# Kernel tuning notes

Hardware: AMD Instinct MI355X
Metric: run time of the kernel (lower is better)

The kernel has to match this reference:

```python
import jax, jax.numpy as jnp
import numpy as np

D_MODEL = 2048
D_FF = 8192
N_HEADS = 16
N_KV_HEADS = 8
HEAD_DIM = D_MODEL // N_HEADS  # 128
R_Q = 64
R_KV = 64
KERNEL_DIM = 64
LN_EPS = 1e-5


def setup_inputs() -> dict:
    key = jax.random.key(0)
    ks = jax.random.split(key, 16)
    s = 0.02
    inp = {
        "x": jax.random.normal(ks[0], (4, 4096, D_MODEL), dtype=jnp.float32),
        # multi-latent low-rank projections (stored as (in, out))
        "W_dq": jax.random.normal(ks[1], (D_MODEL, R_Q), dtype=jnp.float32) * s,
        "W_uq": jax.random.normal(ks[2], (R_Q, N_HEADS * HEAD_DIM), dtype=jnp.float32) * s,
        "W_dkv": jax.random.normal(ks[3], (D_MODEL, R_KV), dtype=jnp.float32) * s,
        "W_uk": jax.random.normal(ks[4], (R_KV, N_KV_HEADS * HEAD_DIM), dtype=jnp.float32) * s,
        "W_uv": jax.random.normal(ks[5], (R_KV, N_KV_HEADS * HEAD_DIM), dtype=jnp.float32) * s,
        # laplacian kernel random features: omega ~ Cauchy (random Fourier features of Laplacian kernel)
        "omega": jax.random.cauchy(ks[6], (HEAD_DIM, KERNEL_DIM), dtype=jnp.float32) * 0.1,
        "W_o": jax.random.normal(ks[7], (N_HEADS * HEAD_DIM, D_MODEL), dtype=jnp.float32) * s,
        "ln1_g": jnp.ones((D_MODEL,), jnp.float32),
        "ln1_b": jnp.zeros((D_MODEL,), jnp.float32),
        "gate_W": jax.random.normal(ks[8], (D_MODEL, D_FF), dtype=jnp.float32) * s,
        "up_W": jax.random.normal(ks[9], (D_MODEL, D_FF), dtype=jnp.float32) * s,
        "down_W": jax.random.normal(ks[10], (D_FF, D_MODEL), dtype=jnp.float32) * s,
        "ln2_g": jnp.ones((D_MODEL,), jnp.float32),
        "ln2_b": jnp.zeros((D_MODEL,), jnp.float32),
    }
    return inp


def _layernorm(x, g, b):
    mu = jnp.mean(x, axis=-1, keepdims=True)
    var = jnp.var(x, axis=-1, keepdims=True)
    return (x - mu) * jax.lax.rsqrt(var + LN_EPS) * g + b


def _phi(x, omega):
    # laplacian-kernel random Fourier feature map: [B,H,S,Dh] -> [B,H,S,2*KERNEL_DIM]
    proj = jnp.einsum("bhsd,dk->bhsk", x, omega)
    scale = 1.0 / jnp.sqrt(jnp.float32(KERNEL_DIM))
    return jnp.concatenate([jnp.cos(proj), jnp.sin(proj)], axis=-1) * scale


def _mlgka_forward(x, W_dq, W_uq, W_dkv, W_uk, W_uv, omega, W_o,
                   ln1_g, ln1_b, gate_W, up_W, down_W, ln2_g, ln2_b):
    B, S, _ = x.shape
    # --- multi-latent (low-rank) Q/KV projections ---
    c_q = jnp.einsum("bsd,dr->bsr", x, W_dq)            # [B,S,r_q]
    q = jnp.einsum("bsr,re->bse", c_q, W_uq)            # [B,S,H*Dh]
    c_kv = jnp.einsum("bsd,dr->bsr", x, W_dkv)          # [B,S,r_kv]
    k = jnp.einsum("bsr,re->bse", c_kv, W_uk)           # [B,S,Hkv*Dh]
    v = jnp.einsum("bsr,re->bse", c_kv, W_uv)           # [B,S,Hkv*Dh]

    q = q.reshape(B, S, N_HEADS, HEAD_DIM).transpose(0, 2, 1, 3)        # [B,H,S,Dh]
    k = k.reshape(B, S, N_KV_HEADS, HEAD_DIM).transpose(0, 2, 1, 3)     # [B,Hkv,S,Dh]
    v = v.reshape(B, S, N_KV_HEADS, HEAD_DIM).transpose(0, 2, 1, 3)

    # GQA: repeat kv heads to match query heads
    rep = N_HEADS // N_KV_HEADS
    k = jnp.repeat(k, rep, axis=1)                                      # [B,H,S,Dh]
    v = jnp.repeat(v, rep, axis=1)

    # --- kernelized (linear) bidirectional attention ---
    phi_q = _phi(q, omega)                                              # [B,H,S,F]
    phi_k = _phi(k, omega)                                              # [B,H,S,F]
    kv = jnp.einsum("bhsf,bhsd->bhfd", phi_k, v)                        # [B,H,F,Dh]
    z = jnp.sum(phi_k, axis=2)                                          # [B,H,F]
    num = jnp.einsum("bhsf,bhfd->bhsd", phi_q, kv)                      # [B,H,S,Dh]
    den = jnp.einsum("bhsf,bhf->bhs", phi_q, z)[..., None]              # [B,H,S,1]
    attn = num / (den + 1e-6)

    attn = attn.transpose(0, 2, 1, 3).reshape(B, S, N_HEADS * HEAD_DIM)
    attn_out = jnp.einsum("bse,ed->bsd", attn, W_o)

    # --- residual + LN, SwiGLU FFN, residual + LN ---
    h = _layernorm(x + attn_out, ln1_g, ln1_b)
    gate = jnp.einsum("bsd,df->bsf", h, gate_W)
    up = jnp.einsum("bsd,df->bsf", h, up_W)
    ffn = jnp.einsum("bsf,fd->bsd", gate * jax.nn.silu(up), down_W)
    return _layernorm(h + ffn, ln2_g, ln2_b)


def reference(x, W_dq, W_uq, W_dkv, W_uk, W_uv, omega, W_o,
              ln1_g, ln1_b, gate_W, up_W, down_W, ln2_g, ln2_b):
    return _mlgka_forward(x, W_dq, W_uq, W_dkv, W_uk, W_uv, omega, W_o,
                          ln1_g, ln1_b, gate_W, up_W, down_W, ln2_g, ln2_b)
```

## Files before the change

kernel.cpp:

```cpp
#include <hip/hip_runtime.h>
#include <stdint.h>
#include <math.h>


typedef __bf16 bf16x8 __attribute__((ext_vector_type(8)));
typedef float f32x4 __attribute__((ext_vector_type(4)));
typedef float f32x2 __attribute__((ext_vector_type(2)));
typedef unsigned short u16x8 __attribute__((ext_vector_type(8)));
typedef unsigned short u16x4 __attribute__((ext_vector_type(4)));

#define DEV __device__ __forceinline__

DEV unsigned short f2b(float f) {
  union { float f; unsigned int u; } v;
  v.f = f;
  unsigned int u = v.u;
  return (unsigned short)((u + 0x7FFFu + ((u >> 16) & 1u)) >> 16);
}
DEV float b2f(unsigned short h) {
  union { unsigned int u; float f; } v;
  v.u = ((unsigned int)h) << 16;
  return v.f;
}

DEV void async16(const void* g, void* l) {
  typedef __attribute__((address_space(1))) unsigned int* gp_t;
  typedef __attribute__((address_space(3))) unsigned int* lp_t;
  __builtin_amdgcn_global_load_lds((gp_t)(g), (lp_t)(l), 16, 0, 0);
}

#define SCHED0() __builtin_amdgcn_sched_barrier(0)
#define BARRIER() do { SCHED0(); __builtin_amdgcn_s_barrier(); SCHED0(); } while (0)
#define LGKM0() do { asm volatile("s_waitcnt lgkmcnt(0)" ::: "memory"); SCHED0(); } while (0)

template <int BN, typename Epi>
DEV void gemm8p(const unsigned short* __restrict__ A,
                const unsigned short* __restrict__ Bt,
                int K, int lda, int ldb, Epi epi) {
  constexpr int CW = BN / 4;
  constexpr int JT = CW / 32;
  constexpr int QBS = CW / 2;
  constexpr int SZB = BN * 64;
  constexpr int BUFB = 2 * 16384 + 2 * SZB;
  constexpr int LB = BN / 128;
  constexpr int VMC = 4 + LB;
  __shared__ alignas(16) char lds[2 * BUFB];

  const int tid = threadIdx.x;
  const int lane = tid & 63;
  const int wave = tid >> 6;
  const int wm = wave >> 2, wn = wave & 3;
  const int ln = lane & 15;
  const int kq2 = ((lane >> 4) & 3) << 4;

  int srA[2], kbA[2], srB[2], kbB[2];
#pragma unroll
  for (int p = 0; p < 2; ++p) {
    int o = (p * 512 + tid) * 16;
    int x = o ^ (((o >> 9) & 1) << 5);
    srA[p] = x >> 7; kbA[p] = (x & 127) >> 1;
  }
#pragma unroll
  for (int p = 0; p < LB; ++p) {
    int o = (p * 512 + tid) * 16;
    int x = o ^ (((o >> 9) & 1) << 5);
    srB[p] = x >> 7; kbB[p] = (x & 127) >> 1;
  }

  const int NT = K >> 6;

  auto stageA = [&](int T, int qa) {
    char* dst = lds + (T & 1) * BUFB + qa * 16384;
    const unsigned short* src = A + T * 64;
#pragma unroll
    for (int p = 0; p < 2; ++p) {
      int r = ((srA[p] >> 6) << 7) | (qa << 6) | (srA[p] & 63);
      async16(src + (size_t)r * lda + kbA[p], dst + (p * 512 + tid) * 16);
    }
  };
  auto stageB = [&](int T, int qb) {
    char* dst = lds + (T & 1) * BUFB + 32768 + qb * SZB;
    const unsigned short* src = Bt + T * 64;
#pragma unroll
    for (int p = 0; p < LB; ++p) {
      int n = (srB[p] / QBS) * CW + qb * QBS + (srB[p] % QBS);
      async16(src + (size_t)n * ldb + kbB[p], dst + (p * 512 + tid) * 16);
    }
  };

  bf16x8 av[4][2], bv[JT][2];
  auto readA = [&](int b, int qa) {
#pragma unroll
    for (int i = 0; i < 4; ++i) {
      int sr = wm * 64 + i * 16 + ln;
      const char* rp = lds + b * BUFB + qa * 16384 + sr * 128;
      int sw = (sr & 4) << 3;
      av[i][0] = *(const bf16x8*)(rp + (kq2 ^ sw));
      av[i][1] = *(const bf16x8*)(rp + ((64 + kq2) ^ sw));
    }
  };
  auto readB = [&](int b, int qb) {
#pragma unroll
    for (int j = 0; j < JT; ++j) {
      int sr = wn * QBS + j * 16 + ln;
      const char* rp = lds + b * BUFB + 32768 + qb * SZB + sr * 128;
      int sw = (sr & 4) << 3;
      bv[j][0] = *(const bf16x8*)(rp + (kq2 ^ sw));
      bv[j][1] = *(const bf16x8*)(rp + ((64 + kq2) ^ sw));
    }
  };

  f32x4 acc[8][2 * JT];
  const f32x4 fz = {0.f, 0.f, 0.f, 0.f};
#pragma unroll
  for (int i = 0; i < 8; ++i)
#pragma unroll
    for (int j = 0; j < 2 * JT; ++j) acc[i][j] = fz;

  auto mf = [&](int qa, int qb) {
#pragma unroll
    for (int tt = 0; tt < 2; ++tt)
#pragma unroll
      for (int i = 0; i < 4; ++i)
#pragma unroll
        for (int j = 0; j < JT; ++j)
          acc[qa * 4 + i][qb * JT + j] = __builtin_amdgcn_mfma_f32_16x16x32_bf16(
              av[i][tt], bv[j][tt], acc[qa * 4 + i][qb * JT + j], 0, 0, 0);
  };

  auto vwait_steady = [&]() {
    if constexpr (VMC == 6) asm volatile("s_waitcnt vmcnt(6)" ::: "memory");
    else                    asm volatile("s_waitcnt vmcnt(5)" ::: "memory");
  };

  stageA(0, 0); stageB(0, 0); stageB(0, 1); stageA(0, 1);
  if (NT > 1) {
    stageA(1, 0); stageB(1, 1); stageA(1, 1);
    vwait_steady();
  } else {
    asm volatile("s_waitcnt vmcnt(0)" ::: "memory");
  }
  BARRIER();

  for (int t = 0; t < NT; ++t) {
    const int b = t & 1;
    readA(b, 0); readB(b, 0);
    if (t + 1 < NT) stageB(t + 1, 0);
    BARRIER(); LGKM0();
    __builtin_amdgcn_s_setprio(1); mf(0, 0); __builtin_amdgcn_s_setprio(0);
    BARRIER();
    readB(b, 1);
    if (t + 2 < NT) stageA(t + 2, 0);
    BARRIER(); LGKM0();
    __builtin_amdgcn_s_setprio(1); mf(0, 1); __builtin_amdgcn_s_setprio(0);
    BARRIER();
    readA(b, 1);
    if (t + 2 < NT) stageB(t + 2, 1);
    BARRIER(); LGKM0();
    __builtin_amdgcn_s_setprio(1); mf(1, 1); __builtin_amdgcn_s_setprio(0);
    BARRIER();
    readB(b, 0);
    if (t + 2 < NT) stageA(t + 2, 1);
    BARRIER(); LGKM0();
    __builtin_amdgcn_s_setprio(1); mf(1, 0); __builtin_amdgcn_s_setprio(0);
    if (t + 2 < NT) vwait_steady();
    else            asm volatile("s_waitcnt vmcnt(0)" ::: "memory");
    BARRIER();
  }

  const int rb = ((lane >> 4) & 3) * 4;
#pragma unroll
  for (int qa = 0; qa < 2; ++qa)
#pragma unroll
    for (int i = 0; i < 4; ++i)
#pragma unroll
      for (int qb = 0; qb < 2; ++qb)
#pragma unroll
        for (int j = 0; j < JT; ++j)
#pragma unroll
          for (int r = 0; r < 4; ++r)
            epi(wm * 128 + qa * 64 + i * 16 + rb + r,
                wn * CW + qb * QBS + j * 16 + ln,
                acc[qa * 4 + i][qb * JT + j][r]);
}

__global__ __launch_bounds__(512) void k_gemm_wo(const unsigned short* __restrict__ A,
                                                 const unsigned short* __restrict__ Bt,
                                                 const float* __restrict__ x,
                                                 unsigned short* __restrict__ y) {
  const int bid = blockIdx.x;
  const int swz = (bid & 7) * 64 + (bid >> 3);
  const int m0 = (swz >> 3) * 256, n0 = (swz & 7) * 256;
  gemm8p<256>(A + (size_t)m0 * 2048, Bt + (size_t)n0 * 2048, 2048, 2048, 2048,
              [=](int r, int cc, float v) {
                size_t idx = (size_t)(m0 + r) * 2048 + n0 + cc;
                y[idx] = f2b(v + x[idx]);
              });
}

__global__ __launch_bounds__(512) void k_gemm_up2(const unsigned short* __restrict__ A,
                                                  const unsigned short* __restrict__ Bt,
                                                  unsigned short* __restrict__ act) {
  const int bid = blockIdx.x;
  const int swz = (bid & 7) * 64 + (bid >> 3);
  const int m0 = (swz >> 5) * 256, n0 = (swz & 31) * 256;
  gemm8p<256>(A + (size_t)m0 * 2048, Bt + (size_t)n0 * 2048, 2048, 2048, 2048,
              [=](int r, int cc, float v) {
                float s = v / (1.f + __expf(-v));
                act[(size_t)(m0 + r) * 8192 + n0 + cc] = f2b(s);
              });
}

__global__ __launch_bounds__(512) void k_gemm_gatem(const unsigned short* __restrict__ A,
                                                    const unsigned short* __restrict__ Bt,
                                                    unsigned short* act) {
  const int bid = blockIdx.x;
  const int swz = (bid & 7) * 64 + (bid >> 3);
  const int m0 = (swz >> 5) * 256, n0 = (swz & 31) * 256;
  gemm8p<256>(A + (size_t)m0 * 2048, Bt + (size_t)n0 * 2048, 2048, 2048, 2048,
              [=](int r, int cc, float v) {
                size_t idx = (size_t)(m0 + r) * 8192 + n0 + cc;
                act[idx] = f2b(v * b2f(act[idx]));
              });
}

__global__ __launch_bounds__(512) void k_gemm_down2(const unsigned short* __restrict__ A,
                                                    const unsigned short* __restrict__ Bt,
                                                    const unsigned short* __restrict__ hbuf,
                                                    float* __restrict__ outc) {
  const int bid = blockIdx.x;
  const int swz = (bid & 7) * 32 + (bid >> 3);
  const int m0 = (swz >> 4) * 256, n0 = (swz & 15) * 128;
  gemm8p<128>(A + (size_t)m0 * 8192, Bt + (size_t)n0 * 8192, 8192, 8192, 8192,
              [=](int r, int cc, float v) {
                size_t idx = (size_t)(m0 + r) * 2048 + n0 + cc;
                outc[idx] = v + b2f(hbuf[idx]);
              });
}

__global__ __launch_bounds__(256) void k_tc(const float* __restrict__ in,
                                            unsigned short* __restrict__ out, int R, int C) {
  __shared__ float tile[64][65];
  const int c0 = blockIdx.x * 64, r0 = blockIdx.y * 64;
  const int tid = threadIdx.x;
#pragma unroll
  for (int p = 0; p < 16; ++p) {
    int l = p * 256 + tid;
    int ir = l >> 6, ic = l & 63;
    tile[ic][ir] = in[(size_t)(r0 + ir) * C + c0 + ic];
  }
  __syncthreads();
#pragma unroll
  for (int p = 0; p < 16; ++p) {
    int l = p * 256 + tid;
    int oc = l >> 6, orr = l & 63;
    out[(size_t)(c0 + oc) * R + r0 + orr] = f2b(tile[oc][orr]);
  }
}

__global__ __launch_bounds__(256) void k_zero(float* __restrict__ p, int n) {
  int i = blockIdx.x * 256 + threadIdx.x;
  if (i < n) p[i] = 0.f;
}

__global__ __launch_bounds__(256) void k_wproj(const float* __restrict__ W_uq,
                                               const float* __restrict__ W_uk,
                                               const float* __restrict__ omega,
                                               float* __restrict__ wqp, float* __restrict__ wkp) {
  const int bi = blockIdx.x;
  const float* W;
  float* outp;
  int ldw, col0;
  if (bi < 16) { W = W_uq; outp = wqp + bi * 4096; ldw = 2048; col0 = bi * 128; }
  else         { W = W_uk; outp = wkp + (bi - 16) * 4096; ldw = 1024; col0 = (bi - 16) * 128; }
  __shared__ float om[128][64];
  const int tid = threadIdx.x;
#pragma unroll
  for (int p = 0; p < 32; ++p) {
    int l = p * 256 + tid;
    om[l >> 6][l & 63] = omega[l];
  }
  __syncthreads();
  const int r = tid >> 2, f0 = (tid & 3) * 16;
  float acc[16];
#pragma unroll
  for (int f = 0; f < 16; ++f) acc[f] = 0.f;
  const float* wrow = W + (size_t)r * ldw + col0;
  for (int d = 0; d < 128; ++d) {
    float w = wrow[d];
#pragma unroll
    for (int f = 0; f < 16; ++f) acc[f] += w * om[d][f0 + f];
  }
#pragma unroll
  for (int f = 0; f < 16; ++f) outp[r * 64 + f0 + f] = acc[f];
}

__global__ __launch_bounds__(256) void k_cgemm(const float* __restrict__ x,
                                               const float* __restrict__ W_dq,
                                               const float* __restrict__ W_dkv,
                                               float* __restrict__ cbuf) {
  __shared__ float xs[64][65];
  __shared__ float wsh[64][128];
  const int tok0 = blockIdx.x * 64;
  const int tid = threadIdx.x;
  const int ty = tid >> 3, tx = tid & 7;
  const int t0 = ty * 2, c0 = tx * 16;
  float acc[2][16];
#pragma unroll
  for (int i = 0; i < 2; ++i)
#pragma unroll
    for (int e = 0; e < 16; ++e) acc[i][e] = 0.f;
  for (int kb = 0; kb < 2048; kb += 64) {
#pragma unroll
    for (int p = 0; p < 16; ++p) {
      int l = p * 256 + tid;
      int tr = l >> 6, kd = l & 63;
      xs[tr][kd] = x[(size_t)(tok0 + tr) * 2048 + kb + kd];
    }
#pragma unroll
    for (int p = 0; p < 32; ++p) {
      int l = p * 256 + tid;
      int kd = l >> 7, c = l & 127;
      wsh[kd][c] = (c < 64) ? W_dq[(size_t)(kb + kd) * 64 + c]
                            : W_dkv[(size_t)(kb + kd) * 64 + (c - 64)];
    }
    __syncthreads();
    for (int kd = 0; kd < 64; ++kd) {
      float a0 = xs[t0][kd], a1 = xs[t0 + 1][kd];
#pragma unroll
      for (int e = 0; e < 16; ++e) {
        float w = wsh[kd][c0 + e];
        acc[0][e] += a0 * w;
        acc[1][e] += a1 * w;
      }
    }
    __syncthreads();
  }
#pragma unroll
  for (int i = 0; i < 2; ++i)
#pragma unroll
    for (int e = 0; e < 16; ++e)
      cbuf[(size_t)(tok0 + t0 + i) * 128 + c0 + e] = acc[i][e];
}

__global__ __launch_bounds__(256) void k_phikz(const float* __restrict__ c,
                                               const float* __restrict__ wkp,
                                               float* __restrict__ phikT,
                                               float* __restrict__ z) {
  const int s0 = blockIdx.x * 64;
  const int bh = blockIdx.y;
  const int b = bh >> 3, hkv = bh & 7;
  __shared__ float ck[64][65];
  __shared__ float wp[64][68];
  const int tid = threadIdx.x;
#pragma unroll
  for (int p = 0; p < 16; ++p) {
    int l = p * 256 + tid;
    int sr = l >> 6, d = l & 63;
    ck[sr][d] = c[(size_t)(b * 4096 + s0 + sr) * 128 + 64 + d];
    wp[sr][d] = wkp[hkv * 4096 + l];
  }
  __syncthreads();
  const int ty = tid & 31, fx = tid >> 5;
  const int f0 = fx * 8, r0 = ty * 2;
  float pr[2][8];
#pragma unroll
  for (int rr = 0; rr < 2; ++rr)
#pragma unroll
    for (int ff = 0; ff < 8; ++ff) pr[rr][ff] = 0.f;
  for (int d = 0; d < 64; ++d) {
    f32x4 w0 = *(const f32x4*)&wp[d][f0];
    f32x4 w1 = *(const f32x4*)&wp[d][f0 + 4];
    float c0v = ck[r0][d], c1v = ck[r0 + 1][d];
#pragma unroll
    for (int e = 0; e < 4; ++e) {
      pr[0][e] += c0v * w0[e]; pr[0][4 + e] += c0v * w1[e];
      pr[1][e] += c1v * w0[e]; pr[1][4 + e] += c1v * w1[e];
    }
  }
  float* obase = phikT + (size_t)bh * 524288 + s0 + r0;
  float zc[8], zs2[8];
#pragma unroll
  for (int ff = 0; ff < 8; ++ff) {
    float sv0, cv0, sv1, cv1;
    __sincosf(pr[0][ff], &sv0, &cv0);
    __sincosf(pr[1][ff], &sv1, &cv1);
    float c0 = cv0 * 0.125f, c1 = cv1 * 0.125f;
    float s0v = sv0 * 0.125f, s1v = sv1 * 0.125f;
    f32x2 co; co[0] = c0; co[1] = c1;
    f32x2 si; si[0] = s0v; si[1] = s1v;
    *(f32x2*)(obase + (size_t)(f0 + ff) * 4096) = co;
    *(f32x2*)(obase + (size_t)(64 + f0 + ff) * 4096) = si;
    zc[ff] = c0 + c1;
    zs2[ff] = s0v + s1v;
  }
#pragma unroll
  for (int off = 16; off; off >>= 1) {
#pragma unroll
    for (int ff = 0; ff < 8; ++ff) {
      zc[ff] += __shfl_down(zc[ff], off);
      zs2[ff] += __shfl_down(zs2[ff], off);
    }
  }
  if (ty == 0) {
#pragma unroll
    for (int ff = 0; ff < 8; ++ff) {
      atomicAdd(&z[bh * 128 + f0 + ff], zc[ff]);
      atomicAdd(&z[bh * 128 + 64 + f0 + ff], zs2[ff]);
    }
  }
}

__global__ __launch_bounds__(256) void k_vf(const float* __restrict__ c,
                                            const float* __restrict__ W_uv,
                                            float* __restrict__ vT) {
  const int s0 = blockIdx.x * 64;
  const int bh = blockIdx.y;
  const int b = bh >> 3, hkv = bh & 7;
  __shared__ float ck[64][65];
  __shared__ float wv[64][132];
  const int tid = threadIdx.x;
#pragma unroll
  for (int p = 0; p < 16; ++p) {
    int l = p * 256 + tid;
    int sr = l >> 6, d = l & 63;
    ck[sr][d] = c[(size_t)(b * 4096 + s0 + sr) * 128 + 64 + d];
  }
#pragma unroll
  for (int p = 0; p < 32; ++p) {
    int l = p * 256 + tid;
    int rr = l >> 7, d = l & 127;
    wv[rr][d] = W_uv[(size_t)rr * 1024 + hkv * 128 + d];
  }
  __syncthreads();
  const int ty = tid & 15, tx = tid >> 4;
  const int r0 = ty * 4, d0 = tx * 8;
  float acc[4][8];
#pragma unroll
  for (int rr = 0; rr < 4; ++rr)
#pragma unroll
    for (int dd = 0; dd < 8; ++dd) acc[rr][dd] = 0.f;
  for (int kk = 0; kk < 64; ++kk) {
    f32x4 w0 = *(const f32x4*)&wv[kk][d0];
    f32x4 w1 = *(const f32x4*)&wv[kk][d0 + 4];
    float cv[4];
#pragma unroll
    for (int rr = 0; rr < 4; ++rr) cv[rr] = ck[r0 + rr][kk];
#pragma unroll
    for (int rr = 0; rr < 4; ++rr)
#pragma unroll
      for (int e = 0; e < 4; ++e) {
        acc[rr][e] += cv[rr] * w0[e];
        acc[rr][4 + e] += cv[rr] * w1[e];
      }
  }
  float* obase = vT + (size_t)bh * 524288 + s0 + r0;
#pragma unroll
  for (int dd = 0; dd < 8; ++dd) {
    f32x4 pv;
    pv[0] = acc[0][dd]; pv[1] = acc[1][dd]; pv[2] = acc[2][dd]; pv[3] = acc[3][dd];
    *(f32x4*)(obase + (size_t)(d0 + dd) * 4096) = pv;
  }
}

__global__ __launch_bounds__(256) void k_kvf2(const float* __restrict__ phikT,
                                              const float* __restrict__ vT,
                                              float* __restrict__ kvf) {
  const int fq = blockIdx.x >> 2, dq = blockIdx.x & 3, bh = blockIdx.y;
  const float* pT = phikT + (size_t)bh * 524288 + (size_t)fq * 32 * 4096;
  const float* vB = vT + (size_t)bh * 524288 + (size_t)dq * 32 * 4096;
  __shared__ float ps[64][33];
  __shared__ float vs[64][33];
  const int tid = threadIdx.x;
  const int fi = tid >> 3, d0 = (tid & 7) * 4;
  f32x4 acc = {0.f, 0.f, 0.f, 0.f};
  for (int ss = 0; ss < 4096; ss += 64) {
#pragma unroll
    for (int p = 0; p < 8; ++p) {
      int l = p * 256 + tid;
      int rr = l >> 6, si = l & 63;
      ps[si][rr] = pT[(size_t)rr * 4096 + ss + si];
      vs[si][rr] = vB[(size_t)rr * 4096 + ss + si];
    }
    __syncthreads();
    for (int si = 0; si < 64; ++si) {
      float pv = ps[si][fi];
#pragma unroll
      for (int j = 0; j < 4; ++j) acc[j] += pv * vs[si][d0 + j];
    }
    __syncthreads();
  }
  float* o = kvf + ((size_t)bh * 128 + fq * 32 + fi) * 128 + dq * 32 + d0;
  *(f32x4*)o = acc;
}

__global__ __launch_bounds__(256) void k_attn2(const float* __restrict__ c,
                                               const float* __restrict__ wqp,
                                               const float* __restrict__ zb,
                                               const float* __restrict__ kvf,
                                               unsigned short* __restrict__ attn) {
  const int s0 = blockIdx.x * 64;
  const int bh = blockIdx.y;
  const int b = bh >> 4, hh = bh & 15;
  const int bhk = (b << 3) + (hh >> 1);
  __shared__ float wq[4096];
  __shared__ float cqt[64][33];
  __shared__ float phl[32][130];
  __shared__ float kvl[128][32];
  __shared__ float zl[128];
  __shared__ float denl[32];
  const int tid = threadIdx.x;
  if (tid < 128) zl[tid] = zb[bhk * 128 + tid];
#pragma unroll
  for (int p = 0; p < 16; ++p) wq[p * 256 + tid] = wqp[hh * 4096 + p * 256 + tid];
  const int fx = tid & 7, ty = tid >> 3;
  const int f0 = fx * 8;
  for (int hf = 0; hf < 2; ++hf) {
    __syncthreads();
#pragma unroll
    for (int p = 0; p < 8; ++p) {
      int l = p * 256 + tid;
      int sr = l >> 6, dd = l & 63;
      cqt[dd][sr] = c[(size_t)(b * 4096 + s0 + hf * 32 + sr) * 128 + dd];
    }
    __syncthreads();
    float pr[8];
#pragma unroll
    for (int ff = 0; ff < 8; ++ff) pr[ff] = 0.f;
    for (int dd = 0; dd < 64; ++dd) {
      f32x4 w0 = *(const f32x4*)(wq + dd * 64 + f0);
      f32x4 w1 = *(const f32x4*)(wq + dd * 64 + f0 + 4);
      float cv = cqt[dd][ty];
#pragma unroll
      for (int e = 0; e < 4; ++e) { pr[e] += cv * w0[e]; pr[4 + e] += cv * w1[e]; }
    }
    float dpart = 0.f;
#pragma unroll
    for (int ff = 0; ff < 8; ++ff) {
      float sv, cv;
      __sincosf(pr[ff], &sv, &cv);
      cv *= 0.125f; sv *= 0.125f;
      phl[ty][f0 + ff] = cv;
      phl[ty][64 + f0 + ff] = sv;
      dpart += cv * zl[f0 + ff] + sv * zl[64 + f0 + ff];
    }
    dpart += __shfl_down(dpart, 4);
    dpart += __shfl_down(dpart, 2);
    dpart += __shfl_down(dpart, 1);
    if (fx == 0) denl[ty] = dpart + 1e-6f;
    __syncthreads();
    for (int dq = 0; dq < 4; ++dq) {
#pragma unroll
      for (int p = 0; p < 16; ++p) {
        int l = p * 256 + tid;
        int f = l >> 5, j = l & 31;
        kvl[f][j] = kvf[(size_t)bhk * 16384 + (size_t)f * 128 + dq * 32 + j];
      }
      __syncthreads();
      const int row = tid >> 3, d0 = (tid & 7) * 4;
      f32x4 acc = {0.f, 0.f, 0.f, 0.f};
      for (int f = 0; f < 128; f += 2) {
        f32x2 pa = *(const f32x2*)&phl[row][f];
        f32x4 k0 = *(const f32x4*)&kvl[f][d0];
        f32x4 k1 = *(const f32x4*)&kvl[f + 1][d0];
#pragma unroll
        for (int j = 0; j < 4; ++j) acc[j] += pa[0] * k0[j] + pa[1] * k1[j];
      }
      const float dn = denl[row];
      u16x4 o4;
#pragma unroll
      for (int j = 0; j < 4; ++j) o4[j] = f2b(acc[j] / dn);
      *(u16x4*)(attn + (size_t)(b * 4096 + s0 + hf * 32 + row) * 2048 + hh * 128 + dq * 32 + d0) = o4;
      __syncthreads();
    }
  }
}

__global__ __launch_bounds__(256) void k_ln_b2b(const unsigned short* __restrict__ in,
                                                const float* __restrict__ g,
                                                const float* __restrict__ bb,
                                                unsigned short* __restrict__ ob) {
  const int row = blockIdx.x;
  const unsigned short* xr = in + (size_t)row * 2048;
  float vals[8], s = 0.f, ss = 0.f;
#pragma unroll
  for (int i = 0; i < 8; ++i) {
    float v = b2f(xr[i * 256 + threadIdx.x]);
    vals[i] = v; s += v; ss += v * v;
  }
#pragma unroll
  for (int off = 32; off; off >>= 1) { s += __shfl_down(s, off); ss += __shfl_down(ss, off); }
  __shared__ float red[8];
  const int wave = threadIdx.x >> 6;
  if ((threadIdx.x & 63) == 0) { red[wave * 2] = s; red[wave * 2 + 1] = ss; }
  __syncthreads();
  float S = red[0] + red[2] + red[4] + red[6];
  float SS = red[1] + red[3] + red[5] + red[7];
  float mu = S * (1.f / 2048.f);
  float var = SS * (1.f / 2048.f) - mu * mu;
  float inv = rsqrtf(var + 1e-5f);
#pragma unroll
  for (int i = 0; i < 8; ++i) {
    int col = i * 256 + threadIdx.x;
    ob[(size_t)row * 2048 + col] = f2b((vals[i] - mu) * inv * g[col] + bb[col]);
  }
}

__global__ __launch_bounds__(256) void k_ln_ip(float* __restrict__ io,
                                               const float* __restrict__ g,
                                               const float* __restrict__ bb) {
  const int row = blockIdx.x;
  float* xr = io + (size_t)row * 2048;
  float vals[8], s = 0.f, ss = 0.f;
#pragma unroll
  for (int i = 0; i < 8; ++i) {
    float v = xr[i * 256 + threadIdx.x];
    vals[i] = v; s += v; ss += v * v;
  }
#pragma unroll
  for (int off = 32; off; off >>= 1) { s += __shfl_down(s, off); ss += __shfl_down(ss, off); }
  __shared__ float red[8];
  const int wave = threadIdx.x >> 6;
  if ((threadIdx.x & 63) == 0) { red[wave * 2] = s; red[wave * 2 + 1] = ss; }
  __syncthreads();
  float S = red[0] + red[2] + red[4] + red[6];
  float SS = red[1] + red[3] + red[5] + red[7];
  float mu = S * (1.f / 2048.f);
  float var = SS * (1.f / 2048.f) - mu * mu;
  float inv = rsqrtf(var + 1e-5f);
#pragma unroll
  for (int i = 0; i < 8; ++i) {
    int col = i * 256 + threadIdx.x;
    xr[col] = (vals[i] - mu) * inv * g[col] + bb[col];
  }
}

extern "C" void kernel_launch(void* const* d_in, const int* in_sizes, int n_in,
                              void* d_out, int out_size, void* d_ws, size_t ws_size,
                              hipStream_t stream) {
  (void)in_sizes; (void)n_in; (void)out_size; (void)ws_size;
  const float* x     = (const float*)d_in[0];
  const float* W_dq  = (const float*)d_in[1];
  const float* W_uq  = (const float*)d_in[2];
  const float* W_dkv = (const float*)d_in[3];
  const float* W_uk  = (const float*)d_in[4];
  const float* W_uv  = (const float*)d_in[5];
  const float* omega = (const float*)d_in[6];
  const float* W_o   = (const float*)d_in[7];
  const float* ln1g  = (const float*)d_in[8];
  const float* ln1b  = (const float*)d_in[9];
  const float* gateW = (const float*)d_in[10];
  const float* upW   = (const float*)d_in[11];
  const float* downW = (const float*)d_in[12];
  const float* ln2g  = (const float*)d_in[13];
  const float* ln2b  = (const float*)d_in[14];
  float* out = (float*)d_out;

  char* w = (char*)d_ws;
  float*          phikTf = (float*)(w);
  float*          vTf    = (float*)(w + 67108864);
  unsigned short* attn   = (unsigned short*)(w + 67108864);
  unsigned short* hb     = (unsigned short*)(w + 67108864);
  unsigned short* gatet  = (unsigned short*)(w);
  unsigned short* upt    = (unsigned short*)(w + 33554432);
  char* C = w + 134217728;
  float*          cbuf = (float*)(C);
  float*          wqp  = (float*)(C + 8388608);
  float*          wkp  = (float*)(C + 8650752);
  float*          zb   = (float*)(C + 8781824);
  float*          kvf  = (float*)(C + 8798208);
  unsigned short* y    = (unsigned short*)(C);
  unsigned short* act  = (unsigned short*)(C);
  unsigned short* wot   = (unsigned short*)(w + 201326592);
  unsigned short* downt = (unsigned short*)(w + 209715200);

  k_zero<<<16, 256, 0, stream>>>(zb, 4096);
  k_wproj<<<24, 256, 0, stream>>>(W_uq, W_uk, omega, wqp, wkp);
  k_tc<<<dim3(32, 32), 256, 0, stream>>>(W_o, wot, 2048, 2048);

  k_cgemm<<<256, 256, 0, stream>>>(x, W_dq, W_dkv, cbuf);

  k_phikz<<<dim3(64, 32), 256, 0, stream>>>(cbuf, wkp, phikTf, zb);
  k_vf<<<dim3(64, 32), 256, 0, stream>>>(cbuf, W_uv, vTf);

  k_kvf2<<<dim3(16, 32), 256, 0, stream>>>(phikTf, vTf, kvf);
  k_attn2<<<dim3(64, 64), 256, 0, stream>>>(cbuf, wqp, zb, kvf, attn);

  k_gemm_wo<<<dim3(512), 512, 0, stream>>>(attn, wot, x, y);
  k_ln_b2b<<<16384, 256, 0, stream>>>(y, ln1g, ln1b, hb);

  k_tc<<<dim3(128, 32), 256, 0, stream>>>(gateW, gatet, 2048, 8192);
  k_tc<<<dim3(128, 32), 256, 0, stream>>>(upW, upt, 2048, 8192);
  k_tc<<<dim3(32, 128), 256, 0, stream>>>(downW, downt, 8192, 2048);

  for (int cix = 0; cix < 4; ++cix) {
    const unsigned short* hbc = hb + (size_t)cix * 4096 * 2048;
    float* outc = out + (size_t)cix * 4096 * 2048;
    k_gemm_up2<<<dim3(512), 512, 0, stream>>>(hbc, upt, act);
    k_gemm_gatem<<<dim3(512), 512, 0, stream>>>(hbc, gatet, act);
    k_gemm_down2<<<dim3(256), 512, 0, stream>>>(act, downt, hbc, outc);
    k_ln_ip<<<4096, 256, 0, stream>>>(outc, ln2g, ln2b);
  }
}
```

Baseline: 3.160 ms.

## Move linear-attention KV and numerator products onto bf16 MFMA GEMMs

Stores phi_k and v as bf16 instead of fp32 and replaces the scalar fp32 kv reduction with a split-K bf16 MFMA GEMM, followed by a reduce-and-transpose kernel. The attention kernel is split in two: one computes phi_q in bf16 plus reciprocal denominators, the other runs the phi_q·kv numerator as an MFMA GEMM with scaling in the epilogue. The aim is to take the attention stage off slow scalar FMA loops and halve intermediate traffic. The cost is extra launches, partial-sum buffers, and bf16 rounding of phi and kv.

```diff
diff --git a/kernel.cpp b/kernel.cpp
--- a/kernel.cpp
+++ b/kernel.cpp
@@ -8,6 +8,7 @@
 typedef float f32x2 __attribute__((ext_vector_type(2)));
 typedef unsigned short u16x8 __attribute__((ext_vector_type(8)));
 typedef unsigned short u16x4 __attribute__((ext_vector_type(4)));
+typedef unsigned short u16x2 __attribute__((ext_vector_type(2)));
 
 #define DEV __device__ __forceinline__
 
@@ -32,6 +33,64 @@
 #define SCHED0() __builtin_amdgcn_sched_barrier(0)
 #define BARRIER() do { SCHED0(); __builtin_amdgcn_s_barrier(); SCHED0(); } while (0)
 #define LGKM0() do { asm volatile("s_waitcnt lgkmcnt(0)" ::: "memory"); SCHED0(); } while (0)
+
+template <typename Epi>
+DEV void gemm_core(const unsigned short* __restrict__ A,
+                   const unsigned short* __restrict__ Bt,
+                   int K, int lda, int ldb, Epi epi) {
+  __shared__ alignas(16) unsigned short As[128 * 64];
+  __shared__ alignas(16) unsigned short Bs[128 * 64];
+  const int tid = threadIdx.x;
+  const int lane = tid & 63;
+  const int wr = ((tid >> 6) >> 1) * 64;
+  const int wc = ((tid >> 6) & 1) * 64;
+  const int ln = lane & 15;
+  const int kq = (lane >> 4) * 8;
+
+  const f32x4 fz = {0.f, 0.f, 0.f, 0.f};
+  f32x4 acc[4][4];
+#pragma unroll
+  for (int i = 0; i < 4; ++i)
+#pragma unroll
+    for (int j = 0; j < 4; ++j) acc[i][j] = fz;
+
+  for (int kb = 0; kb < K; kb += 64) {
+#pragma unroll
+    for (int c = 0; c < 4; ++c) {
+      int o = (c * 256 + tid) * 16;
+      int row = o >> 7;
+      int ke = (o & 127) >> 1;
+      async16(A + (size_t)row * lda + kb + ke, (void*)(As + (o >> 1)));
+      async16(Bt + (size_t)row * ldb + kb + ke, (void*)(Bs + (o >> 1)));
+    }
+    __syncthreads();
+#pragma unroll
+    for (int t = 0; t < 2; ++t) {
+      const int kk = t * 32 + kq;
+      bf16x8 av[4], bv[4];
+#pragma unroll
+      for (int i = 0; i < 4; ++i)
+        av[i] = *(const bf16x8*)(As + (wr + i * 16 + ln) * 64 + kk);
+#pragma unroll
+      for (int j = 0; j < 4; ++j)
+        bv[j] = *(const bf16x8*)(Bs + (wc + j * 16 + ln) * 64 + kk);
+#pragma unroll
+      for (int i = 0; i < 4; ++i)
+#pragma unroll
+        for (int j = 0; j < 4; ++j)
+          acc[i][j] = __builtin_amdgcn_mfma_f32_16x16x32_bf16(av[i], bv[j], acc[i][j], 0, 0, 0);
+    }
+    __syncthreads();
+  }
+  const int rb = (lane >> 4) * 4;
+#pragma unroll
+  for (int i = 0; i < 4; ++i)
+#pragma unroll
+    for (int j = 0; j < 4; ++j)
+#pragma unroll
+      for (int r = 0; r < 4; ++r)
+        epi(wr + i * 16 + rb + r, wc + j * 16 + ln, acc[i][j][r]);
+}
 
 template <int BN, typename Epi>
 DEV void gemm8p(const unsigned short* __restrict__ A,
@@ -345,7 +404,7 @@
 
 __global__ __launch_bounds__(256) void k_phikz(const float* __restrict__ c,
                                                const float* __restrict__ wkp,
-                                               float* __restrict__ phikT,
+                                               unsigned short* __restrict__ phikT,
                                                float* __restrict__ z) {
   const int s0 = blockIdx.x * 64;
   const int bh = blockIdx.y;
@@ -378,7 +437,7 @@
       pr[1][e] += c1v * w0[e]; pr[1][4 + e] += c1v * w1[e];
     }
   }
-  float* obase = phikT + (size_t)bh * 524288 + s0 + r0;
+  unsigned short* obase = phikT + (size_t)bh * 524288 + s0 + r0;
   float zc[8], zs2[8];
 #pragma unroll
   for (int ff = 0; ff < 8; ++ff) {
@@ -387,10 +446,10 @@
     __sincosf(pr[1][ff], &sv1, &cv1);
     float c0 = cv0 * 0.125f, c1 = cv1 * 0.125f;
     float s0v = sv0 * 0.125f, s1v = sv1 * 0.125f;
-    f32x2 co; co[0] = c0; co[1] = c1;
-    f32x2 si; si[0] = s0v; si[1] = s1v;
-    *(f32x2*)(obase + (size_t)(f0 + ff) * 4096) = co;
-    *(f32x2*)(obase + (size_t)(64 + f0 + ff) * 4096) = si;
+    u16x2 co; co[0] = f2b(c0); co[1] = f2b(c1);
+    u16x2 si; si[0] = f2b(s0v); si[1] = f2b(s1v);
+    *(u16x2*)(obase + (size_t)(f0 + ff) * 4096) = co;
+    *(u16x2*)(obase + (size_t)(64 + f0 + ff) * 4096) = si;
     zc[ff] = c0 + c1;
     zs2[ff] = s0v + s1v;
   }
@@ -413,7 +472,7 @@
 
 __global__ __launch_bounds__(256) void k_vf(const float* __restrict__ c,
                                             const float* __restrict__ W_uv,
-                                            float* __restrict__ vT) {
+                                            unsigned short* __restrict__ vT) {
   const int s0 = blockIdx.x * 64;
   const int bh = blockIdx.y;
   const int b = bh >> 3, hkv = bh & 7;
@@ -454,61 +513,63 @@
         acc[rr][4 + e] += cv[rr] * w1[e];
       }
   }
-  float* obase = vT + (size_t)bh * 524288 + s0 + r0;
+  unsigned short* obase = vT + (size_t)bh * 524288 + s0 + r0;
 #pragma unroll
   for (int dd = 0; dd < 8; ++dd) {
-    f32x4 pv;
-    pv[0] = acc[0][dd]; pv[1] = acc[1][dd]; pv[2] = acc[2][dd]; pv[3] = acc[3][dd];
-    *(f32x4*)(obase + (size_t)(d0 + dd) * 4096) = pv;
-  }
-}
-
-__global__ __launch_bounds__(256) void k_kvf2(const float* __restrict__ phikT,
-                                              const float* __restrict__ vT,
-                                              float* __restrict__ kvf) {
-  const int fq = blockIdx.x >> 2, dq = blockIdx.x & 3, bh = blockIdx.y;
-  const float* pT = phikT + (size_t)bh * 524288 + (size_t)fq * 32 * 4096;
-  const float* vB = vT + (size_t)bh * 524288 + (size_t)dq * 32 * 4096;
-  __shared__ float ps[64][33];
-  __shared__ float vs[64][33];
-  const int tid = threadIdx.x;
-  const int fi = tid >> 3, d0 = (tid & 7) * 4;
-  f32x4 acc = {0.f, 0.f, 0.f, 0.f};
-  for (int ss = 0; ss < 4096; ss += 64) {
-#pragma unroll
-    for (int p = 0; p < 8; ++p) {
-      int l = p * 256 + tid;
-      int rr = l >> 6, si = l & 63;
-      ps[si][rr] = pT[(size_t)rr * 4096 + ss + si];
-      vs[si][rr] = vB[(size_t)rr * 4096 + ss + si];
-    }
-    __syncthreads();
-    for (int si = 0; si < 64; ++si) {
-      float pv = ps[si][fi];
-#pragma unroll
-      for (int j = 0; j < 4; ++j) acc[j] += pv * vs[si][d0 + j];
-    }
-    __syncthreads();
-  }
-  float* o = kvf + ((size_t)bh * 128 + fq * 32 + fi) * 128 + dq * 32 + d0;
-  *(f32x4*)o = acc;
-}
-
-__global__ __launch_bounds__(256) void k_attn2(const float* __restrict__ c,
-                                               const float* __restrict__ wqp,
-                                               const float* __restrict__ zb,
-                                               const float* __restrict__ kvf,
-                                               unsigned short* __restrict__ attn) {
+    u16x4 pv;
+    pv[0] = f2b(acc[0][dd]); pv[1] = f2b(acc[1][dd]);
+    pv[2] = f2b(acc[2][dd]); pv[3] = f2b(acc[3][dd]);
+    *(u16x4*)(obase + (size_t)(d0 + dd) * 4096) = pv;
+  }
+}
+
+__global__ __launch_bounds__(256) void k_kvg(const unsigned short* __restrict__ phikT,
+                                             const unsigned short* __restrict__ vT,
+                                             float* __restrict__ kvp) {
+  const int kc = blockIdx.x, bh = blockIdx.y;
+  gemm_core(phikT + (size_t)bh * 524288 + kc * 512,
+            vT + (size_t)bh * 524288 + kc * 512, 512, 4096, 4096,
+            [=](int r, int cc, float v) {
+              kvp[((size_t)(kc * 32 + bh) * 128 + r) * 128 + cc] = v;
+            });
+}
+
+__global__ __launch_bounds__(256) void k_kvredt(const float* __restrict__ kvp,
+                                                unsigned short* __restrict__ kvbT) {
+  const int fx0 = blockIdx.x * 64, dx0 = blockIdx.y * 64, bhk = blockIdx.z;
+  __shared__ float tile[64][65];
+  const int tid = threadIdx.x;
+#pragma unroll
+  for (int p = 0; p < 16; ++p) {
+    int l = p * 256 + tid;
+    int fr = l >> 6, dc = l & 63;
+    float s = 0.f;
+#pragma unroll
+    for (int kc = 0; kc < 8; ++kc)
+      s += kvp[(size_t)kc * 524288 + ((size_t)bhk * 128 + fx0 + fr) * 128 + dx0 + dc];
+    tile[dc][fr] = s;
+  }
+  __syncthreads();
+#pragma unroll
+  for (int p = 0; p < 16; ++p) {
+    int l = p * 256 + tid;
+    int dr = l >> 6, fc = l & 63;
+    kvbT[((size_t)bhk * 128 + dx0 + dr) * 128 + fx0 + fc] = f2b(tile[dr][fc]);
+  }
+}
+
+__global__ __launch_bounds__(256) void k_phiq(const float* __restrict__ c,
+                                              const float* __restrict__ wqp,
+                                              const float* __restrict__ zb,
+                                              unsigned short* __restrict__ phiq,
+                                              float* __restrict__ rden) {
   const int s0 = blockIdx.x * 64;
   const int bh = blockIdx.y;
   const int b = bh >> 4, hh = bh & 15;
   const int bhk = (b << 3) + (hh >> 1);
   __shared__ float wq[4096];
   __shared__ float cqt[64][33];
-  __shared__ float phl[32][130];
-  __shared__ float kvl[128][32];
   __shared__ float zl[128];
-  __shared__ float denl[32];
   const int tid = threadIdx.x;
   if (tid < 128) zl[tid] = zb[bhk * 128 + tid];
 #pragma unroll
@@ -535,45 +596,39 @@
       for (int e = 0; e < 4; ++e) { pr[e] += cv * w0[e]; pr[4 + e] += cv * w1[e]; }
     }
     float dpart = 0.f;
+    u16x8 pc, ps;
 #pragma unroll
     for (int ff = 0; ff < 8; ++ff) {
       float sv, cv;
       __sincosf(pr[ff], &sv, &cv);
       cv *= 0.125f; sv *= 0.125f;
-      phl[ty][f0 + ff] = cv;
-      phl[ty][64 + f0 + ff] = sv;
+      pc[ff] = f2b(cv); ps[ff] = f2b(sv);
       dpart += cv * zl[f0 + ff] + sv * zl[64 + f0 + ff];
     }
+    unsigned short* ob = phiq + ((size_t)bh * 4096 + s0 + hf * 32 + ty) * 128;
+    *(u16x8*)(ob + f0) = pc;
+    *(u16x8*)(ob + 64 + f0) = ps;
     dpart += __shfl_down(dpart, 4);
     dpart += __shfl_down(dpart, 2);
     dpart += __shfl_down(dpart, 1);
-    if (fx == 0) denl[ty] = dpart + 1e-6f;
-    __syncthreads();
-    for (int dq = 0; dq < 4; ++dq) {
-#pragma unroll
-      for (int p = 0; p < 16; ++p) {
-        int l = p * 256 + tid;
-        int f = l >> 5, j = l & 31;
-        kvl[f][j] = kvf[(size_t)bhk * 16384 + (size_t)f * 128 + dq * 32 + j];
-      }
-      __syncthreads();
-      const int row = tid >> 3, d0 = (tid & 7) * 4;
-      f32x4 acc = {0.f, 0.f, 0.f, 0.f};
-      for (int f = 0; f < 128; f += 2) {
-        f32x2 pa = *(const f32x2*)&phl[row][f];
-        f32x4 k0 = *(const f32x4*)&kvl[f][d0];
-        f32x4 k1 = *(const f32x4*)&kvl[f + 1][d0];
-#pragma unroll
-        for (int j = 0; j < 4; ++j) acc[j] += pa[0] * k0[j] + pa[1] * k1[j];
-      }
-      const float dn = denl[row];
-      u16x4 o4;
-#pragma unroll
-      for (int j = 0; j < 4; ++j) o4[j] = f2b(acc[j] / dn);
-      *(u16x4*)(attn + (size_t)(b * 4096 + s0 + hf * 32 + row) * 2048 + hh * 128 + dq * 32 + d0) = o4;
-      __syncthreads();
-    }
-  }
+    if (fx == 0) rden[(size_t)bh * 4096 + s0 + hf * 32 + ty] = 1.f / (dpart + 1e-6f);
+  }
+}
+
+__global__ __launch_bounds__(256) void k_num(const unsigned short* __restrict__ phiq,
+                                             const unsigned short* __restrict__ kvbT,
+                                             const float* __restrict__ rden,
+                                             unsigned short* __restrict__ attn) {
+  const int m0 = blockIdx.x * 128;
+  const int bh = blockIdx.y;
+  const int b = bh >> 4, hh = bh & 15;
+  const int bhk = (b << 3) + (hh >> 1);
+  const float* rd = rden + (size_t)bh * 4096 + m0;
+  gemm_core(phiq + ((size_t)bh * 4096 + m0) * 128, kvbT + (size_t)bhk * 16384,
+            128, 128, 128,
+            [=](int r, int cc, float v) {
+              attn[(size_t)(b * 4096 + m0 + r) * 2048 + hh * 128 + cc] = f2b(v * rd[r]);
+            });
 }
 
 __global__ __launch_bounds__(256) void k_ln_b2b(const unsigned short* __restrict__ in,
@@ -657,18 +712,21 @@
   float* out = (float*)d_out;
 
   char* w = (char*)d_ws;
-  float*          phikTf = (float*)(w);
-  float*          vTf    = (float*)(w + 67108864);
-  unsigned short* attn   = (unsigned short*)(w + 67108864);
-  unsigned short* hb     = (unsigned short*)(w + 67108864);
-  unsigned short* gatet  = (unsigned short*)(w);
-  unsigned short* upt    = (unsigned short*)(w + 33554432);
+  unsigned short* phikT = (unsigned short*)(w);
+  unsigned short* phiqb = (unsigned short*)(w);
+  unsigned short* vT    = (unsigned short*)(w + 67108864);
+  unsigned short* attn  = (unsigned short*)(w + 67108864);
+  unsigned short* hb    = (unsigned short*)(w + 67108864);
+  unsigned short* gatet = (unsigned short*)(w);
+  unsigned short* upt   = (unsigned short*)(w + 33554432);
   char* C = w + 134217728;
   float*          cbuf = (float*)(C);
   float*          wqp  = (float*)(C + 8388608);
   float*          wkp  = (float*)(C + 8650752);
   float*          zb   = (float*)(C + 8781824);
-  float*          kvf  = (float*)(C + 8798208);
+  float*          rden = (float*)(C + 8798208);
+  unsigned short* kvbT = (unsigned short*)(C + 9846784);
+  float*          kvp  = (float*)(C + 10895360);
   unsigned short* y    = (unsigned short*)(C);
   unsigned short* act  = (unsigned short*)(C);
   unsigned short* wot   = (unsigned short*)(w + 201326592);
@@ -680,11 +738,13 @@
 
   k_cgemm<<<256, 256, 0, stream>>>(x, W_dq, W_dkv, cbuf);
 
-  k_phikz<<<dim3(64, 32), 256, 0, stream>>>(cbuf, wkp, phikTf, zb);
-  k_vf<<<dim3(64, 32), 256, 0, stream>>>(cbuf, W_uv, vTf);
-
-  k_kvf2<<<dim3(16, 32), 256, 0, stream>>>(phikTf, vTf, kvf);
-  k_attn2<<<dim3(64, 64), 256, 0, stream>>>(cbuf, wqp, zb, kvf, attn);
+  k_phikz<<<dim3(64, 32), 256, 0, stream>>>(cbuf, wkp, phikT, zb);
+  k_vf<<<dim3(64, 32), 256, 0, stream>>>(cbuf, W_uv, vT);
+
+  k_kvg<<<dim3(8, 32), 256, 0, stream>>>(phikT, vT, kvp);
+  k_kvredt<<<dim3(2, 2, 32), 256, 0, stream>>>(kvp, kvbT);
+  k_phiq<<<dim3(64, 64), 256, 0, stream>>>(cbuf, wqp, zb, phiqb, rden);
+  k_num<<<dim3(32, 64), 256, 0, stream>>>(phiqb, kvbT, rden, attn);
 
   k_gemm_wo<<<dim3(512), 512, 0, stream>>>(attn, wot, x, y);
   k_ln_b2b<<<16384, 256, 0, stream>>>(y, ln1g, ln1b, hb);
```

New measurement: 2.847 ms. 9.9% less time.
